# Optimization experiments

Hardware: AMD Instinct MI355X
Metric: run time of the kernel (lower is better)

The kernel has to match this reference:

```python
import jax, jax.numpy as jnp
import numpy as np

B, T, F, H = 64, 512, 1024, 1024

def setup_inputs() -> dict:
    key = jax.random.key(0)
    ks = jax.random.split(key, 13)
    def w(k, shape):
        return jax.random.normal(k, shape, dtype=jnp.float32) * 0.02
    inp = {"x": jax.random.normal(ks[0], (B, T, F), dtype=jnp.float32)}
    names = ["i", "f", "g", "o"]
    for j, n in enumerate(names):
        inp[f"U_{n}"] = w(ks[1 + 3 * j], (F, H))
        inp[f"V_{n}"] = w(ks[2 + 3 * j], (H, H))
        inp[f"b_{n}"] = w(ks[3 + 3 * j], (H,))
    return inp


def reference(x, U_i, V_i, b_i, U_f, V_f, b_f, U_g, V_g, b_g, U_o, V_o, b_o):
    batch = x.shape[0]
    hid = V_i.shape[0]
    # Concatenate the 4 gate projections into single GEMMs (same math, fused).
    U = jnp.concatenate([U_i, U_f, U_g, U_o], axis=1)  # [F, 4H]
    V = jnp.concatenate([V_i, V_f, V_g, V_o], axis=1)  # [H, 4H]
    b = jnp.concatenate([b_i, b_f, b_g, b_o], axis=0)  # [4H]
    # Precompute input contribution for all timesteps in one big GEMM.
    xU = jnp.einsum("btf,fk->btk", x, U) + b           # [B, T, 4H]
    xU_t = jnp.swapaxes(xU, 0, 1)                       # [T, B, 4H]

    def step(carry, xu):
        h, c = carry
        z = xu + h @ V                                  # [B, 4H]
        zi, zf, zg, zo = jnp.split(z, 4, axis=-1)
        i_t = jax.nn.sigmoid(zi)
        f_t = jax.nn.sigmoid(zf)
        g_t = jnp.tanh(zg)
        o_t = jnp.tanh(zo)  # NOTE: source uses tanh (not sigmoid) for output gate
        c = f_t * c + i_t * g_t
        h = o_t * jnp.tanh(c)
        return (h, c), None

    h0 = jnp.zeros((batch, hid), dtype=x.dtype)
    c0 = jnp.zeros((batch, hid), dtype=x.dtype)
    (h_t, c_t), _ = jax.lax.scan(step, (h0, c0), xU_t)
    return h_t
```

## Files before the change

kernel.cpp:

```cpp
#include <hip/hip_runtime.h>

using u16 = unsigned short;
using u32 = unsigned int;
using u64 = unsigned long long;
using bf16x8 = __attribute__((ext_vector_type(8))) short;
using f16x8  = __attribute__((ext_vector_type(8))) _Float16;
using f32x4  = __attribute__((ext_vector_type(4))) float;
using u32x4  = __attribute__((ext_vector_type(4))) unsigned int;

static constexpr size_t XU_OFF = 0;
static constexpr size_t XU_BYTES = (size_t)512 * 64 * 4096 * 2;
static constexpr size_t XB_OFF = XU_OFF + XU_BYTES;
static constexpr size_t XB_BYTES = (size_t)64 * 512 * 1024 * 2;
static constexpr size_t UT_OFF = XB_OFF + XB_BYTES;
static constexpr size_t WT_BYTES = (size_t)4096 * 1024 * 2;
static constexpr size_t VT_OFF = UT_OFF + WT_BYTES;
static constexpr size_t BP_OFF = VT_OFF + WT_BYTES;
static constexpr size_t BP_BYTES = 4096 * 4;
static constexpr size_t HT_PLANE = (size_t)2 * 4 * 16 * 1024 * 2;
static constexpr size_t HHI_OFF = BP_OFF + BP_BYTES;
static constexpr size_t FLAG_OFF = HHI_OFF + HT_PLANE;
static constexpr size_t FLAG_BYTES = 4096;

__device__ __forceinline__ float bf2f(u32 u) {
    return __uint_as_float(u << 16);
}
__device__ __forceinline__ u16 f2bf(float f) {
    u32 u = __float_as_uint(f);
    u32 r = (u + 0x7FFFu + ((u >> 16) & 1u)) >> 16;
    return (u16)r;
}
__device__ __forceinline__ u16 f2h(float f) {
    _Float16 x = (_Float16)f;
    union { _Float16 h; u16 u; } cv;
    cv.h = x;
    return cv.u;
}

__device__ __forceinline__ float fast_sigmoid(float x) {
    return __builtin_amdgcn_rcpf(1.f + __expf(-x));
}
__device__ __forceinline__ float fast_tanh(float x) {
    return 1.f - 2.f * __builtin_amdgcn_rcpf(1.f + __expf(2.f * x));
}

__device__ __forceinline__ u32x4 load16_uc(const u16* p) {
    u32x4 v;
    asm volatile("global_load_dwordx4 %0, %1, off sc0 sc1"
                 : "=v"(v)
                 : "v"(p));
    return v;
}

__device__ __forceinline__ void store16_wt(u16* p, u32x4 v) {
    asm volatile("global_store_dwordx4 %0, %1, off sc0 sc1"
                 :: "v"(p), "v"(v) : "memory");
}

__device__ __forceinline__ void wait_vm4(int j, u32x4& a) {
    switch (j) {
    case 0:  asm volatile("s_waitcnt vmcnt(3)" : "+v"(a)); break;
    case 1:  asm volatile("s_waitcnt vmcnt(2)" : "+v"(a)); break;
    case 2:  asm volatile("s_waitcnt vmcnt(1)" : "+v"(a)); break;
    default: asm volatile("s_waitcnt vmcnt(0)" : "+v"(a)); break;
    }
}

__device__ __forceinline__ void gld16(const u16* g, u16* l) {
    __builtin_amdgcn_global_load_lds((const __attribute__((address_space(1))) void*)g,
                                     (__attribute__((address_space(3))) void*)l,
                                     16, 0, 0);
}

__device__ __forceinline__ void wait_chunk(const u32* cnt, int c) {
    for (;;) {
        u32 v = __hip_atomic_load(cnt + c, __ATOMIC_RELAXED, __HIP_MEMORY_SCOPE_AGENT);
        if (v >= 2048u) break;
        __builtin_amdgcn_s_sleep(8);
    }
    asm volatile("" ::: "memory");
}

__global__ void cvt_x_kernel(const float4* __restrict__ x, uint2* __restrict__ xb) {
    int i = blockIdx.x * 256 + threadIdx.x;
#pragma unroll
    for (int k = 0; k < 8; ++k) {
        int idx = i + k * 1048576;
        float4 v = x[idx];
        uint2 o;
        o.x = (u32)f2bf(v.x) | ((u32)f2bf(v.y) << 16);
        o.y = (u32)f2bf(v.z) | ((u32)f2bf(v.w) << 16);
        xb[idx] = o;
    }
}

__global__ void repack_kernel(const float* U0, const float* U1, const float* U2, const float* U3,
                              const float* V0, const float* V1, const float* V2, const float* V3,
                              u16* UT, u16* VT) {
    __shared__ u16 tile[64][65];
    int bx  = blockIdx.x;
    int mat = bx >> 8;
    int rem = bx & 255;
    int tf = rem >> 4, th = rem & 15;
    int f0 = tf * 64, h0 = th * 64;
    const float* srcs[8] = {U0, U1, U2, U3, V0, V1, V2, V3};
    const float* s = srcs[mat];
    u16* d = (mat < 4) ? UT : VT;
    bool isU = (mat < 4);
    int g = mat & 3;
    int c = threadIdx.x & 63;
    int r = threadIdx.x >> 6;
#pragma unroll
    for (int i = 0; i < 16; ++i) {
        int fr = r + i * 4;
        float v = s[(size_t)(f0 + fr) * 1024 + h0 + c];
        tile[fr][c] = isU ? f2bf(v) : f2h(v);
    }
    __syncthreads();
#pragma unroll
    for (int i = 0; i < 16; ++i) {
        int hcl = r + i * 4;
        d[(size_t)((h0 + hcl) * 4 + g) * 1024 + f0 + c] = tile[c][hcl];
    }
}

__global__ void bias_kernel(const float* b0, const float* b1, const float* b2, const float* b3,
                            float* bp) {
    int n = blockIdx.x * 256 + threadIdx.x;
    int g = n & 3, hc = n >> 2;
    const float* bs[4] = {b0, b1, b2, b3};
    bp[n] = bs[g][hc];
}

__device__ __forceinline__ void gemm_tile(int tau,
        const u16* __restrict__ xb, const u16* __restrict__ UT,
        const float* __restrict__ bp, u16* __restrict__ xu,
        u16* As, u16* Bs, u16* Cs, u32* cnt) {
    int tc = tau >> 11, rem = tau & 2047;
    int b = rem >> 5, nt = rem & 31, mt = b * 4 + tc;
    int tid = threadIdx.x;
    int lane = tid & 63, wv = tid >> 6;
    int wm = wv >> 2, wn = wv & 3;
    int l15 = lane & 15, quad = lane >> 4;

    int idr = tid >> 2, idk = (tid & 3) * 8;
    const u16* aS = xb + (size_t)(mt * 128 + idr) * 1024 + idk;
    const u16* bS = UT + (size_t)(nt * 128 + idr) * 1024 + idk;
    u16* aD = As + (size_t)tid * 8;
    u16* bD = Bs + (size_t)tid * 8;

    f32x4 acc[4][2];
#pragma unroll
    for (int i = 0; i < 4; ++i)
#pragma unroll
        for (int j = 0; j < 2; ++j) acc[i][j] = f32x4{0.f, 0.f, 0.f, 0.f};

    float biasv[2];
#pragma unroll
    for (int j = 0; j < 2; ++j) biasv[j] = bp[nt * 128 + wn * 32 + j * 16 + l15];

    for (int k0 = 0; k0 < 1024; k0 += 32) {
        gld16(aS + k0, aD);
        gld16(bS + k0, bD);
        __syncthreads();
        bf16x8 af[4], bfv[2];
#pragma unroll
        for (int i = 0; i < 4; ++i)
            af[i] = *(const bf16x8*)(As + (size_t)(wm * 64 + i * 16 + l15) * 32 + quad * 8);
#pragma unroll
        for (int j = 0; j < 2; ++j)
            bfv[j] = *(const bf16x8*)(Bs + (size_t)(wn * 32 + j * 16 + l15) * 32 + quad * 8);
#pragma unroll
        for (int i = 0; i < 4; ++i)
#pragma unroll
            for (int j = 0; j < 2; ++j)
                acc[i][j] = __builtin_amdgcn_mfma_f32_16x16x32_bf16(af[i], bfv[j], acc[i][j], 0, 0, 0);
        __syncthreads();
    }

#pragma unroll
    for (int i = 0; i < 4; ++i)
#pragma unroll
        for (int j = 0; j < 2; ++j)
#pragma unroll
            for (int rg = 0; rg < 4; ++rg)
                Cs[(size_t)(wm * 64 + i * 16 + quad * 4 + rg) * 136 + wn * 32 + j * 16 + l15] =
                    f2bf(acc[i][j][rg] + biasv[j]);
    __syncthreads();

#pragma unroll
    for (int p = 0; p < 4; ++p) {
        int id = p * 512 + tid;
        int row = id >> 4, q = id & 15;
        u32x4 v = *(const u32x4*)(Cs + (size_t)row * 136 + q * 8);
        int gr = mt * 128 + row;
        int t_i = gr & 511, b_i = gr >> 9;
        store16_wt(xu + (((size_t)(t_i * 64 + b_i)) << 12) + nt * 128 + q * 8, v);
    }
    asm volatile("s_waitcnt vmcnt(0)" ::: "memory");
    __syncthreads();
    if (tid == 0)
        __hip_atomic_fetch_add(cnt + tc, 1u, __ATOMIC_RELAXED, __HIP_MEMORY_SCOPE_AGENT);
}

__global__ void __launch_bounds__(512, 2) lstm_fused_kernel(
        const u16* __restrict__ xb, const u16* __restrict__ UT,
        const float* __restrict__ bp, u16* __restrict__ xu,
        const u16* __restrict__ VT, u16* hhi, u32* flags, u32* cnt,
        float* __restrict__ out) {
    __shared__ u16 As[128 * 32];
    __shared__ u16 Bs[128 * 32];
    __shared__ u16 Cs[128 * 136];
    __shared__ float zs[8][16][132];

    int bx = blockIdx.x;

    for (int p = 0; p < 8; ++p)
        gemm_tile(bx * 8 + p, xb, UT, bp, xu, As, Bs, Cs, cnt);

    if (bx >= 128) {
        int gid = bx - 128;
        for (int p = 0; p < 48; ++p)
            gemm_tile(2048 + p * 128 + gid, xb, UT, bp, xu, As, Bs, Cs, cnt);
        return;
    }

    int g  = bx & 3;
    int cb = bx >> 2;
    int tid = threadIdx.x;
    int lane = tid & 63, wv = tid >> 6;
    int l15 = lane & 15, quad = lane >> 4;
    int r  = tid >> 5;
    int hc = tid & 31;

    f16x8 vfrag[8][4];
    {
        const u16* vb = VT + ((size_t)(cb * 128 + l15) * 1024) + wv * 128 + quad * 8;
#pragma unroll
        for (int nt = 0; nt < 8; ++nt)
#pragma unroll
            for (int j = 0; j < 4; ++j)
                vfrag[nt][j] = *(const f16x8*)(vb + (size_t)nt * 16 * 1024 + j * 32);
    }

    u32* gflags = flags + g * 64;
    int myp = 4 * wv + (lane & 3);

    float c = 0.f;
    float h = 0.f;

    wait_chunk(cnt, 0);
    uint2 xraw = *(const uint2*)(xu + ((size_t)(g * 16 + r) << 12) + cb * 128 + hc * 4);

    for (int t = 0; t < 512; ++t) {
        f32x4 acc[8];
#pragma unroll
        for (int nt = 0; nt < 8; ++nt) acc[nt] = f32x4{0.f, 0.f, 0.f, 0.f};

        if (t) {
            for (;;) {
                u32 f = __hip_atomic_load(gflags + myp, __ATOMIC_RELAXED,
                                          __HIP_MEMORY_SCOPE_AGENT);
                if (__ballot(f >= (u32)t) == ~0ull) break;
                __builtin_amdgcn_s_sleep(1);
            }
            asm volatile("" ::: "memory");

            const u16* hB = hhi + (((size_t)(t & 1) * 4 + g) * 16 + l15) * 1024
                          + wv * 128 + quad * 8;
            u32x4 hv[4];
#pragma unroll
            for (int j = 0; j < 4; ++j)
                hv[j] = load16_uc(hB + j * 32);
#pragma unroll
            for (int j = 0; j < 4; ++j) {
                wait_vm4(j, hv[j]);
                union { u32x4 q; f16x8 v; } ah;
                ah.q = hv[j];
#pragma unroll
                for (int nt = 0; nt < 8; ++nt)
                    acc[nt] = __builtin_amdgcn_mfma_f32_16x16x32_f16(ah.v, vfrag[nt][j], acc[nt], 0, 0, 0);
            }
        }

#pragma unroll
        for (int nt = 0; nt < 8; ++nt)
#pragma unroll
            for (int rg = 0; rg < 4; ++rg)
                zs[wv][quad * 4 + rg][nt * 16 + l15] = acc[nt][rg];
        __syncthreads();

        float4 s = {0.f, 0.f, 0.f, 0.f};
#pragma unroll
        for (int w = 0; w < 8; ++w) {
            float4 v = *(const float4*)&zs[w][r][hc * 4];
            s.x += v.x; s.y += v.y; s.z += v.z; s.w += v.w;
        }
        float z0 = s.x + bf2f(xraw.x & 0xFFFFu);
        float z1 = s.y + bf2f(xraw.x >> 16);
        float z2 = s.z + bf2f(xraw.y & 0xFFFFu);
        float z3 = s.w + bf2f(xraw.y >> 16);

        float it_ = fast_sigmoid(z0);
        float ft_ = fast_sigmoid(z1);
        float gt_ = fast_tanh(z2);
        float ot_ = fast_tanh(z3);
        c = ft_ * c + it_ * gt_;
        h = ot_ * fast_tanh(c);

        if (t == 511) break;

        size_t sidx = (((size_t)((t + 1) & 1) * 4 + g) * 16 + r) * 1024 + cb * 32 + hc;
        __hip_atomic_store(hhi + sidx, f2h(h), __ATOMIC_RELAXED,
                           __HIP_MEMORY_SCOPE_AGENT);
        asm volatile("s_waitcnt vmcnt(0)" ::: "memory");
        __syncthreads();
        if (tid == 0)
            __hip_atomic_store(gflags + cb, (u32)(t + 1), __ATOMIC_RELAXED,
                               __HIP_MEMORY_SCOPE_AGENT);

        if (((t + 1) & 127) == 0) wait_chunk(cnt, (t + 1) >> 7);
        xraw = *(const uint2*)(xu + ((size_t)((t + 1) * 64 + g * 16 + r) << 12) + cb * 128 + hc * 4);
    }

    out[(size_t)(g * 16 + r) * 1024 + cb * 32 + hc] = h;
}

extern "C" void kernel_launch(void* const* d_in, const int* in_sizes, int n_in,
                              void* d_out, int out_size, void* d_ws, size_t ws_size,
                              hipStream_t stream) {
    char* ws = (char*)d_ws;
    const float* x = (const float*)d_in[0];
    const float *U[4], *V[4], *b[4];
    for (int g = 0; g < 4; ++g) {
        U[g] = (const float*)d_in[1 + 3 * g];
        V[g] = (const float*)d_in[2 + 3 * g];
        b[g] = (const float*)d_in[3 + 3 * g];
    }
    u16*   xu = (u16*)(ws + XU_OFF);
    u16*   xb = (u16*)(ws + XB_OFF);
    u16*   UT = (u16*)(ws + UT_OFF);
    u16*   VT = (u16*)(ws + VT_OFF);
    float* bp = (float*)(ws + BP_OFF);
    u16*   hhi = (u16*)(ws + HHI_OFF);
    u32*   flags = (u32*)(ws + FLAG_OFF);
    u32*   cnt = (u32*)(ws + FLAG_OFF + 2048);
    float* out = (float*)d_out;

    hipMemsetAsync(ws + FLAG_OFF, 0, FLAG_BYTES, stream);

    cvt_x_kernel<<<4096, 256, 0, stream>>>((const float4*)x, (uint2*)xb);
    repack_kernel<<<2048, 256, 0, stream>>>(U[0], U[1], U[2], U[3],
                                            V[0], V[1], V[2], V[3], UT, VT);
    bias_kernel<<<16, 256, 0, stream>>>(b[0], b[1], b[2], b[3], bp);

    void* args[] = {(void*)&xb, (void*)&UT, (void*)&bp, (void*)&xu,
                    (void*)&VT, (void*)&hhi, (void*)&flags, (void*)&cnt,
                    (void*)&out};
    hipLaunchCooperativeKernel((const void*)lstm_fused_kernel, dim3(256), dim3(512),
                               args, 0, stream);
}
```

Before: 2.192 ms.

## Fold x conversion, weight repack, bias and flag reset into cooperative kernel

Moves the memset, x-to-bf16 conversion, U/V transpose-repack and bias interleave into the prologue of the persistent cooperative LSTM kernel, separated by a grid-wide sync. This removes four extra launches and their gaps. The xU stores also gain a nontemporal hint. In exchange, the preprocessing runs on only 256 blocks, with half the threads idle during repack, and adds a grid barrier.

```diff
diff --git a/kernel.cpp b/kernel.cpp
--- a/kernel.cpp
+++ b/kernel.cpp
@@ -1,4 +1,5 @@
 #include <hip/hip_runtime.h>
+#include <hip/hip_cooperative_groups.h>
 
 using u16 = unsigned short;
 using u32 = unsigned int;
@@ -20,7 +21,6 @@
 static constexpr size_t HT_PLANE = (size_t)2 * 4 * 16 * 1024 * 2;
 static constexpr size_t HHI_OFF = BP_OFF + BP_BYTES;
 static constexpr size_t FLAG_OFF = HHI_OFF + HT_PLANE;
-static constexpr size_t FLAG_BYTES = 4096;
 
 __device__ __forceinline__ float bf2f(u32 u) {
     return __uint_as_float(u << 16);
@@ -53,7 +53,7 @@
 }
 
 __device__ __forceinline__ void store16_wt(u16* p, u32x4 v) {
-    asm volatile("global_store_dwordx4 %0, %1, off sc0 sc1"
+    asm volatile("global_store_dwordx4 %0, %1, off sc0 sc1 nt"
                  :: "v"(p), "v"(v) : "memory");
 }
 
@@ -79,57 +79,6 @@
         __builtin_amdgcn_s_sleep(8);
     }
     asm volatile("" ::: "memory");
-}
-
-__global__ void cvt_x_kernel(const float4* __restrict__ x, uint2* __restrict__ xb) {
-    int i = blockIdx.x * 256 + threadIdx.x;
-#pragma unroll
-    for (int k = 0; k < 8; ++k) {
-        int idx = i + k * 1048576;
-        float4 v = x[idx];
-        uint2 o;
-        o.x = (u32)f2bf(v.x) | ((u32)f2bf(v.y) << 16);
-        o.y = (u32)f2bf(v.z) | ((u32)f2bf(v.w) << 16);
-        xb[idx] = o;
-    }
-}
-
-__global__ void repack_kernel(const float* U0, const float* U1, const float* U2, const float* U3,
-                              const float* V0, const float* V1, const float* V2, const float* V3,
-                              u16* UT, u16* VT) {
-    __shared__ u16 tile[64][65];
-    int bx  = blockIdx.x;
-    int mat = bx >> 8;
-    int rem = bx & 255;
-    int tf = rem >> 4, th = rem & 15;
-    int f0 = tf * 64, h0 = th * 64;
-    const float* srcs[8] = {U0, U1, U2, U3, V0, V1, V2, V3};
-    const float* s = srcs[mat];
-    u16* d = (mat < 4) ? UT : VT;
-    bool isU = (mat < 4);
-    int g = mat & 3;
-    int c = threadIdx.x & 63;
-    int r = threadIdx.x >> 6;
-#pragma unroll
-    for (int i = 0; i < 16; ++i) {
-        int fr = r + i * 4;
-        float v = s[(size_t)(f0 + fr) * 1024 + h0 + c];
-        tile[fr][c] = isU ? f2bf(v) : f2h(v);
-    }
-    __syncthreads();
-#pragma unroll
-    for (int i = 0; i < 16; ++i) {
-        int hcl = r + i * 4;
-        d[(size_t)((h0 + hcl) * 4 + g) * 1024 + f0 + c] = tile[c][hcl];
-    }
-}
-
-__global__ void bias_kernel(const float* b0, const float* b1, const float* b2, const float* b3,
-                            float* bp) {
-    int n = blockIdx.x * 256 + threadIdx.x;
-    int g = n & 3, hc = n >> 2;
-    const float* bs[4] = {b0, b1, b2, b3};
-    bp[n] = bs[g][hc];
 }
 
 __device__ __forceinline__ void gemm_tile(int tau,
@@ -204,16 +153,90 @@
 }
 
 __global__ void __launch_bounds__(512, 2) lstm_fused_kernel(
-        const u16* __restrict__ xb, const u16* __restrict__ UT,
-        const float* __restrict__ bp, u16* __restrict__ xu,
-        const u16* __restrict__ VT, u16* hhi, u32* flags, u32* cnt,
-        float* __restrict__ out) {
+        const float* __restrict__ x,
+        const float* U0, const float* V0, const float* b0,
+        const float* U1, const float* V1, const float* b1,
+        const float* U2, const float* V2, const float* b2,
+        const float* U3, const float* V3, const float* b3,
+        char* __restrict__ ws, float* __restrict__ out) {
     __shared__ u16 As[128 * 32];
     __shared__ u16 Bs[128 * 32];
     __shared__ u16 Cs[128 * 136];
     __shared__ float zs[8][16][132];
 
+    u16*   xb  = (u16*)(ws + XB_OFF);
+    u16*   UT  = (u16*)(ws + UT_OFF);
+    u16*   VT  = (u16*)(ws + VT_OFF);
+    float* bp  = (float*)(ws + BP_OFF);
+    u16*   xu  = (u16*)(ws + XU_OFF);
+    u16*   hhi = (u16*)(ws + HHI_OFF);
+    u32*   flags = (u32*)(ws + FLAG_OFF);
+    u32*   cnt   = (u32*)(ws + FLAG_OFF + 2048);
+
     int bx = blockIdx.x;
+    int tid = threadIdx.x;
+
+    if (bx == 0) {
+        __hip_atomic_store(flags + tid, 0u, __ATOMIC_RELAXED, __HIP_MEMORY_SCOPE_AGENT);
+        __hip_atomic_store(flags + 512 + tid, 0u, __ATOMIC_RELAXED, __HIP_MEMORY_SCOPE_AGENT);
+    }
+    if (bx == 1) {
+        const float* bsrc[4] = {b0, b1, b2, b3};
+#pragma unroll
+        for (int it = 0; it < 8; ++it) {
+            int n = it * 512 + tid;
+            bp[n] = bsrc[n & 3][n >> 2];
+        }
+    }
+    {
+        const float4* x4 = (const float4*)x;
+        uint2* xb4 = (uint2*)xb;
+        int t0 = bx * 512 + tid;
+#pragma unroll 4
+        for (int k = 0; k < 64; ++k) {
+            int idx = t0 + k * 131072;
+            float4 v = x4[idx];
+            uint2 o;
+            o.x = (u32)f2bf(v.x) | ((u32)f2bf(v.y) << 16);
+            o.y = (u32)f2bf(v.z) | ((u32)f2bf(v.w) << 16);
+            xb4[idx] = o;
+        }
+    }
+    {
+        u16* tile = Cs;
+        const float* srcs[8] = {U0, U1, U2, U3, V0, V1, V2, V3};
+        for (int vb = 0; vb < 8; ++vb) {
+            int vbx = bx * 8 + vb;
+            int mat = vbx >> 8, rem = vbx & 255;
+            int tf = rem >> 4, th = rem & 15;
+            int f0 = tf * 64, h0 = th * 64;
+            const float* s = srcs[mat];
+            u16* d = (mat < 4) ? UT : VT;
+            bool isU = (mat < 4);
+            int gg = mat & 3;
+            if (tid < 256) {
+                int cc = tid & 63, rr = tid >> 6;
+#pragma unroll
+                for (int i = 0; i < 16; ++i) {
+                    int fr = rr + i * 4;
+                    float v = s[(size_t)(f0 + fr) * 1024 + h0 + cc];
+                    tile[fr * 65 + cc] = isU ? f2bf(v) : f2h(v);
+                }
+            }
+            __syncthreads();
+            if (tid < 256) {
+                int cc = tid & 63, rr = tid >> 6;
+#pragma unroll
+                for (int i = 0; i < 16; ++i) {
+                    int hcl = rr + i * 4;
+                    d[(size_t)((h0 + hcl) * 4 + gg) * 1024 + f0 + cc] = tile[cc * 65 + hcl];
+                }
+            }
+            __syncthreads();
+        }
+    }
+    __threadfence();
+    cooperative_groups::this_grid().sync();
 
     for (int p = 0; p < 8; ++p)
         gemm_tile(bx * 8 + p, xb, UT, bp, xu, As, Bs, Cs, cnt);
@@ -227,7 +250,6 @@
 
     int g  = bx & 3;
     int cb = bx >> 2;
-    int tid = threadIdx.x;
     int lane = tid & 63, wv = tid >> 6;
     int l15 = lane & 15, quad = lane >> 4;
     int r  = tid >> 5;
@@ -337,26 +359,14 @@
         V[g] = (const float*)d_in[2 + 3 * g];
         b[g] = (const float*)d_in[3 + 3 * g];
     }
-    u16*   xu = (u16*)(ws + XU_OFF);
-    u16*   xb = (u16*)(ws + XB_OFF);
-    u16*   UT = (u16*)(ws + UT_OFF);
-    u16*   VT = (u16*)(ws + VT_OFF);
-    float* bp = (float*)(ws + BP_OFF);
-    u16*   hhi = (u16*)(ws + HHI_OFF);
-    u32*   flags = (u32*)(ws + FLAG_OFF);
-    u32*   cnt = (u32*)(ws + FLAG_OFF + 2048);
     float* out = (float*)d_out;
 
-    hipMemsetAsync(ws + FLAG_OFF, 0, FLAG_BYTES, stream);
-
-    cvt_x_kernel<<<4096, 256, 0, stream>>>((const float4*)x, (uint2*)xb);
-    repack_kernel<<<2048, 256, 0, stream>>>(U[0], U[1], U[2], U[3],
-                                            V[0], V[1], V[2], V[3], UT, VT);
-    bias_kernel<<<16, 256, 0, stream>>>(b[0], b[1], b[2], b[3], bp);
-
-    void* args[] = {(void*)&xb, (void*)&UT, (void*)&bp, (void*)&xu,
-                    (void*)&VT, (void*)&hhi, (void*)&flags, (void*)&cnt,
-                    (void*)&out};
+    void* args[] = {(void*)&x,
+                    (void*)&U[0], (void*)&V[0], (void*)&b[0],
+                    (void*)&U[1], (void*)&V[1], (void*)&b[1],
+                    (void*)&U[2], (void*)&V[2], (void*)&b[2],
+                    (void*)&U[3], (void*)&V[3], (void*)&b[3],
+                    (void*)&ws, (void*)&out};
     hipLaunchCooperativeKernel((const void*)lstm_fused_kernel, dim3(256), dim3(512),
                                args, 0, stream);
 }
```

After: 2.529 ms. +15.4%, slower.
